# Performance work log

Hardware: AMD Instinct MI355X
Metric: run time of the kernel (lower is better)

## Reference

```python
import jax, jax.numpy as jnp
import numpy as np
from itertools import product

D = 128      # full-resolution voxel grid extent
DP = 64      # pooled grid extent (stride 2)
M = 131072   # number of pooled (output) voxels
CH = 2       # children per pooled cell
N = M * CH   # number of input active voxels = 262144
EPS = 1e-5


def _build_maps():
    rng = np.random.default_rng(0)
    plin = rng.choice(DP ** 3, size=M, replace=False).astype(np.int64)
    px = plin // (DP * DP); py = (plin // DP) % DP; pz = plin % DP
    pcoords = np.stack([px, py, pz], 1)                      # [M,3]
    off8 = np.array(list(product([0, 1], repeat=3)), np.int64)   # [8,3]
    sel = np.argsort(rng.random((M, 8)), 1)[:, :CH]          # pick 2 of 8 children
    coords = (pcoords[:, None, :] * 2 + off8[sel]).reshape(-1, 3)  # [N,3]

    def make_lookup(c, d):
        lin = (c[:, 0] * d + c[:, 1]) * d + c[:, 2]
        order = np.argsort(lin); slin = lin[order]
        def lookup(q):
            inb = np.all((q >= 0) & (q < d), 1)
            ql = (q[:, 0] * d + q[:, 1]) * d + q[:, 2]
            pos = np.searchsorted(slin, ql)
            pos_c = np.clip(pos, 0, len(slin) - 1)
            found = inb & (slin[pos_c] == ql)
            return np.where(found, order[pos_c], -1).astype(np.int32)
        return lookup

    lk_full = make_lookup(coords, D)
    lk_pool = make_lookup(pcoords, DP)
    off27 = np.array(list(product([-1, 0, 1], repeat=3)), np.int64)  # [27,3]
    nbr1 = np.stack([lk_full(coords + o) for o in off27])            # [27,N]
    pool_map = np.stack([lk_full(pcoords * 2 + o) for o in off8])    # [8,M]
    nbr2 = np.stack([lk_pool(pcoords + o) for o in off27])           # [27,M]
    return nbr1, pool_map, nbr2


def setup_inputs() -> dict:
    nbr1, pool_map, nbr2 = _build_maps()
    key = jax.random.key(0)
    k1, k2, k3, k4 = jax.random.split(key, 4)
    feats = jax.random.normal(k1, (N, 3), jnp.float32)
    # kaiming-ish scaling over fan_in = 27*Cin
    W1 = jax.random.normal(k2, (27, 3, 64), jnp.float32) * np.sqrt(2.0 / (27 * 3))
    W2 = jax.random.normal(k3, (27, 64, 64), jnp.float32) * np.sqrt(2.0 / (27 * 64))
    W3 = jax.random.normal(k4, (27, 64, 128), jnp.float32) * np.sqrt(2.0 / (27 * 64))
    return {"feats": feats, "W1": W1, "W2": W2, "W3": W3,
            "nbr1": jnp.asarray(nbr1), "pool_map": jnp.asarray(pool_map),
            "nbr2": jnp.asarray(nbr2)}


def sparse_conv(x, W, nbr):
    """Gather-GEMM-scatter sparse conv. x:[Nin,Cin], W:[K,Cin,Cout], nbr:[K,Nout]."""
    out = jnp.zeros((nbr.shape[1], W.shape[-1]), x.dtype)
    for k in range(W.shape[0]):           # fixed small loop over 27 kernel offsets
        idx = nbr[k]
        m = (idx >= 0)
        g = x[jnp.where(m, idx, 0)] * m[:, None].astype(x.dtype)  # [Nout,Cin]
        out = out + g @ W[k]
    return out


def inst_norm(x):
    mu = jnp.mean(x, axis=0, keepdims=True)
    var = jnp.var(x, axis=0, keepdims=True)
    return (x - mu) / jnp.sqrt(var + EPS)


def max_pool(x, pool_map):
    out = jnp.full((pool_map.shape[1], x.shape[1]), -jnp.inf, x.dtype)
    for o in range(pool_map.shape[0]):    # 8 pooling offsets
        idx = pool_map[o]
        m = (idx >= 0)
        g = jnp.where(m[:, None], x[jnp.where(m, idx, 0)], -jnp.inf)
        out = jnp.maximum(out, g)
    return out


def reference(feats, W1, W2, W3, nbr1, pool_map, nbr2):
    x = jax.nn.relu(inst_norm(sparse_conv(feats, W1, nbr1)))  # [N,64]
    x = jax.nn.relu(inst_norm(sparse_conv(x, W2, nbr1)))      # [N,64]
    x = max_pool(x, pool_map)                                  # [M,64]
    x = jax.nn.relu(inst_norm(sparse_conv(x, W3, nbr2)))      # [M,128]
    return x
```

## Files before the change

kernel.cpp:

```cpp
#include <hip/hip_runtime.h>
#include <hip/hip_bf16.h>

#define N_FULL 262144
#define M_POOL 131072

typedef __attribute__((ext_vector_type(4))) float f32x4;
typedef __attribute__((ext_vector_type(8))) short bf16x8;
typedef __attribute__((ext_vector_type(8))) unsigned short u16x8;

static __device__ __forceinline__ unsigned short f2b(float f) {
    __hip_bfloat16 b = __float2bfloat16(f);
    return *reinterpret_cast<unsigned short*>(&b);
}
static __device__ __forceinline__ float b2f(unsigned short u) {
    unsigned int x = ((unsigned int)u) << 16;
    return __uint_as_float(x);
}

static __device__ __forceinline__ void gll16(const void* g, void* l) {
    __builtin_amdgcn_global_load_lds(
        (const __attribute__((address_space(1))) void*)g,
        (__attribute__((address_space(3))) void*)l, 16, 0, 0);
}

template<int CT, int NPT>
__global__ __launch_bounds__(256) void pack_w_kernel(const float* __restrict__ W,
                                                     unsigned short* __restrict__ Wp) {
    int i = blockIdx.x * 256 + threadIdx.x;
    const int total = NPT * 2 * CT * 64 * 8;
    if (i >= total) return;
    int j = i & 7;
    int l = (i >> 3) & 63;
    int t = (i >> 9) % CT;
    int q = (i / (512 * CT)) & 1;
    int k = i / (1024 * CT);
    int cin = q * 32 + (l >> 4) * 8 + j;
    int cout = t * 16 + (l & 15);
    float v = (k < 27) ? W[(k * 64 + cin) * (CT * 16) + cout] : 0.f;
    Wp[i] = f2b(v);
}

__global__ __launch_bounds__(256) void pack_w1_kernel(const float* __restrict__ W1,
                                                      unsigned short* __restrict__ Wp) {
    int i = blockIdx.x * 256 + threadIdx.x;
    const int total = 7 * 4 * 64 * 8;
    if (i >= total) return;
    int j = i & 7;
    int l = (i >> 3) & 63;
    int t = (i >> 9) & 3;
    int kb = i >> 11;
    int tap = kb * 4 + (l >> 4);
    float v = 0.f;
    if (tap < 27 && j < 3) v = W1[(tap * 3 + j) * 64 + t * 16 + (l & 15)];
    Wp[i] = f2b(v);
}

__global__ __launch_bounds__(256) void conv1_mfma_kernel(const float* __restrict__ feats,
                                                         const unsigned short* __restrict__ Wp,
                                                         const int* __restrict__ nbr,
                                                         unsigned short* __restrict__ Y,
                                                         float* __restrict__ sums, int R) {
    __shared__ unsigned short lw[7 * 2048];
    __shared__ float psum[4][64], psq[4][64];
    const int tid = threadIdx.x;
    const int wave = tid >> 6;
    const int lane = tid & 63;
    const int l16 = lane & 15;
    const int lq = lane >> 4;
    const int rowbase = blockIdx.x * 128 + wave * 32;

    {
        const char* gsrc = (const char*)Wp;
        char* lbase = (char*)lw;
        #pragma unroll
        for (int c = 0; c < 7; ++c) {
            int off = (wave * 7 + c) * 1024;
            gll16(gsrc + off + lane * 16, lbase + off);
        }
    }
    int idx[7][2];
    #pragma unroll
    for (int g = 0; g < 7; ++g) {
        int tap = g * 4 + lq;
        #pragma unroll
        for (int s = 0; s < 2; ++s)
            idx[g][s] = (tap < 27) ? nbr[(size_t)tap * R + rowbase + s * 16 + l16] : -1;
    }
    __syncthreads();

    f32x4 acc[2][4];
    #pragma unroll
    for (int s = 0; s < 2; ++s)
        #pragma unroll
        for (int t = 0; t < 4; ++t)
            #pragma unroll
            for (int g = 0; g < 4; ++g) acc[s][t][g] = 0.f;
    bf16x8 zf;
    #pragma unroll
    for (int j = 0; j < 8; ++j) zf[j] = 0;

    bf16x8 af[7][2];
    #pragma unroll
    for (int g = 0; g < 7; ++g)
        #pragma unroll
        for (int s = 0; s < 2; ++s) {
            af[g][s] = zf;
            int ic = idx[g][s];
            if (ic >= 0) {
                af[g][s][0] = (short)f2b(feats[ic * 3 + 0]);
                af[g][s][1] = (short)f2b(feats[ic * 3 + 1]);
                af[g][s][2] = (short)f2b(feats[ic * 3 + 2]);
            }
        }
    #pragma unroll
    for (int g = 0; g < 7; ++g) {
        #pragma unroll
        for (int t = 0; t < 4; ++t) {
            bf16x8 bfr = *reinterpret_cast<const bf16x8*>(&lw[g * 2048 + t * 512 + lane * 8]);
            #pragma unroll
            for (int s = 0; s < 2; ++s)
                acc[s][t] = __builtin_amdgcn_mfma_f32_16x16x32_bf16(af[g][s], bfr, acc[s][t], 0, 0, 0);
        }
    }
    #pragma unroll
    for (int t = 0; t < 4; ++t) {
        float s1 = 0.f, s2 = 0.f;
        #pragma unroll
        for (int s = 0; s < 2; ++s)
            #pragma unroll
            for (int g = 0; g < 4; ++g) {
                float v = acc[s][t][g];
                s1 += v; s2 += v * v;
                Y[(size_t)(rowbase + s * 16 + lq * 4 + g) * 64 + t * 16 + l16] = f2b(v);
            }
        s1 += __shfl_xor(s1, 16); s2 += __shfl_xor(s2, 16);
        s1 += __shfl_xor(s1, 32); s2 += __shfl_xor(s2, 32);
        if (lq == 0) { psum[wave][t * 16 + l16] = s1; psq[wave][t * 16 + l16] = s2; }
    }
    __syncthreads();
    if (tid < 64) {
        float s1 = 0.f, s2 = 0.f;
        #pragma unroll
        for (int w = 0; w < 4; ++w) { s1 += psum[w][tid]; s2 += psq[w][tid]; }
        atomicAdd(&sums[tid], s1);
        atomicAdd(&sums[64 + tid], s2);
    }
}

template<int CT, int TCH, int NPT>
__global__ __launch_bounds__(256) void conv_mfma_kernel(const unsigned short* __restrict__ X,
                                                        const unsigned short* __restrict__ Wp,
                                                        const int* __restrict__ nbr,
                                                        unsigned short* __restrict__ Y,
                                                        float* __restrict__ sums, int Nout) {
    constexpr int C = CT * 16;
    constexpr int NPH = NPT / TCH;
    constexpr int TAPB = 2 * CT * 512;
    __shared__ unsigned short lw[TCH * TAPB];
    __shared__ float psum[4][C], psq[4][C];
    const int tid = threadIdx.x;
    const int wave = tid >> 6;
    const int lane = tid & 63;
    const int l16 = lane & 15;
    const int lq = lane >> 4;
    const int rowbase = blockIdx.x * 128 + wave * 32;

    f32x4 acc[2][CT];
    #pragma unroll
    for (int s = 0; s < 2; ++s)
        #pragma unroll
        for (int t = 0; t < CT; ++t)
            #pragma unroll
            for (int g = 0; g < 4; ++g) acc[s][t][g] = 0.f;
    bf16x8 zf;
    #pragma unroll
    for (int j = 0; j < 8; ++j) zf[j] = 0;

    int idxp[TCH][2];
    #pragma unroll
    for (int t = 0; t < TCH; ++t)
        #pragma unroll
        for (int s = 0; s < 2; ++s)
            idxp[t][s] = nbr[(size_t)t * Nout + rowbase + s * 16 + l16];

    for (int ph = 0; ph < NPH; ++ph) {
        if (ph) __syncthreads();
        {
            const char* gseg = (const char*)Wp + (size_t)ph * TCH * TAPB * 2;
            char* lbase = (char*)lw;
            const int woff = wave * (TCH * TAPB * 2 / 4);
            #pragma unroll
            for (int c = 0; c < TCH * CT / 2; ++c) {
                int off = woff + c * 1024;
                gll16(gseg + off + lane * 16, lbase + off);
            }
        }
        bf16x8 af[TCH][2][2];
        #pragma unroll
        for (int t = 0; t < TCH; ++t)
            #pragma unroll
            for (int s = 0; s < 2; ++s) {
                int ic = idxp[t][s];
                #pragma unroll
                for (int q = 0; q < 2; ++q) af[t][s][q] = zf;
                if (ic >= 0) {
                    #pragma unroll
                    for (int q = 0; q < 2; ++q)
                        af[t][s][q] = *reinterpret_cast<const bf16x8*>(
                            X + (size_t)ic * 64 + q * 32 + lq * 8);
                }
            }
        int idxn[TCH][2];
        #pragma unroll
        for (int t = 0; t < TCH; ++t) {
            int tap = (ph + 1) * TCH + t;
            #pragma unroll
            for (int s = 0; s < 2; ++s)
                idxn[t][s] = (tap < 27) ? nbr[(size_t)tap * Nout + rowbase + s * 16 + l16] : -1;
        }
        __syncthreads();
        #pragma unroll
        for (int t = 0; t < TCH; ++t) {
            #pragma unroll
            for (int q = 0; q < 2; ++q) {
                #pragma unroll
                for (int tt = 0; tt < CT; ++tt) {
                    bf16x8 bfr = *reinterpret_cast<const bf16x8*>(
                        &lw[t * TAPB + (q * CT + tt) * 512 + lane * 8]);
                    #pragma unroll
                    for (int s = 0; s < 2; ++s)
                        acc[s][tt] = __builtin_amdgcn_mfma_f32_16x16x32_bf16(
                            af[t][s][q], bfr, acc[s][tt], 0, 0, 0);
                }
            }
        }
        #pragma unroll
        for (int t = 0; t < TCH; ++t)
            #pragma unroll
            for (int s = 0; s < 2; ++s) idxp[t][s] = idxn[t][s];
    }
    #pragma unroll
    for (int t = 0; t < CT; ++t) {
        float s1 = 0.f, s2 = 0.f;
        #pragma unroll
        for (int s = 0; s < 2; ++s)
            #pragma unroll
            for (int g = 0; g < 4; ++g) {
                float v = acc[s][t][g];
                s1 += v; s2 += v * v;
                Y[(size_t)(rowbase + s * 16 + lq * 4 + g) * C + t * 16 + l16] = f2b(v);
            }
        s1 += __shfl_xor(s1, 16); s2 += __shfl_xor(s2, 16);
        s1 += __shfl_xor(s1, 32); s2 += __shfl_xor(s2, 32);
        if (lq == 0) { psum[wave][t * 16 + l16] = s1; psq[wave][t * 16 + l16] = s2; }
    }
    __syncthreads();
    if (tid < C) {
        float s1 = 0.f, s2 = 0.f;
        #pragma unroll
        for (int w = 0; w < 4; ++w) { s1 += psum[w][tid]; s2 += psq[w][tid]; }
        atomicAdd(&sums[tid], s1);
        atomicAdd(&sums[C + tid], s2);
    }
}

template<int C>
__global__ __launch_bounds__(256) void norm_bf16_kernel(const unsigned short* __restrict__ Y,
                                                        const float* __restrict__ sums,
                                                        unsigned short* __restrict__ Xb, int R) {
    __shared__ float lmu[C], lrs[C];
    if (threadIdx.x < C) {
        float m = sums[threadIdx.x] / (float)R;
        float v = sums[C + threadIdx.x] / (float)R - m * m;
        lmu[threadIdx.x] = m;
        lrs[threadIdx.x] = rsqrtf(fmaxf(v, 0.f) + 1e-5f);
    }
    __syncthreads();
    const int total = R * C / 8;
    for (int i = blockIdx.x * 256 + threadIdx.x; i < total; i += gridDim.x * 256) {
        u16x8 v = reinterpret_cast<const u16x8*>(Y)[i];
        int cb = (i * 8) & (C - 1);
        u16x8 o;
        #pragma unroll
        for (int j = 0; j < 8; ++j) {
            float f = b2f(v[j]);
            o[j] = f2b(fmaxf((f - lmu[cb + j]) * lrs[cb + j], 0.f));
        }
        reinterpret_cast<u16x8*>(Xb)[i] = o;
    }
}

template<int C>
__global__ __launch_bounds__(256) void norm_f32_kernel(const unsigned short* __restrict__ Y,
                                                       const float* __restrict__ sums,
                                                       float* __restrict__ Out, int R) {
    __shared__ float lmu[C], lrs[C];
    if (threadIdx.x < C) {
        float m = sums[threadIdx.x] / (float)R;
        float v = sums[C + threadIdx.x] / (float)R - m * m;
        lmu[threadIdx.x] = m;
        lrs[threadIdx.x] = rsqrtf(fmaxf(v, 0.f) + 1e-5f);
    }
    __syncthreads();
    const int total = R * C / 8;
    for (int i = blockIdx.x * 256 + threadIdx.x; i < total; i += gridDim.x * 256) {
        u16x8 v = reinterpret_cast<const u16x8*>(Y)[i];
        int cb = (i * 8) & (C - 1);
        float4 o0, o1;
        o0.x = fmaxf((b2f(v[0]) - lmu[cb + 0]) * lrs[cb + 0], 0.f);
        o0.y = fmaxf((b2f(v[1]) - lmu[cb + 1]) * lrs[cb + 1], 0.f);
        o0.z = fmaxf((b2f(v[2]) - lmu[cb + 2]) * lrs[cb + 2], 0.f);
        o0.w = fmaxf((b2f(v[3]) - lmu[cb + 3]) * lrs[cb + 3], 0.f);
        o1.x = fmaxf((b2f(v[4]) - lmu[cb + 4]) * lrs[cb + 4], 0.f);
        o1.y = fmaxf((b2f(v[5]) - lmu[cb + 5]) * lrs[cb + 5], 0.f);
        o1.z = fmaxf((b2f(v[6]) - lmu[cb + 6]) * lrs[cb + 6], 0.f);
        o1.w = fmaxf((b2f(v[7]) - lmu[cb + 7]) * lrs[cb + 7], 0.f);
        reinterpret_cast<float4*>(Out)[i * 2] = o0;
        reinterpret_cast<float4*>(Out)[i * 2 + 1] = o1;
    }
}

__global__ __launch_bounds__(256) void pool_norm_kernel(const unsigned short* __restrict__ Y2,
                                                        const int* __restrict__ pmap,
                                                        const float* __restrict__ sums,
                                                        unsigned short* __restrict__ Xp,
                                                        int M, int R) {
    __shared__ float lmu[64], lrs[64];
    if (threadIdx.x < 64) {
        float m = sums[threadIdx.x] / (float)R;
        float v = sums[64 + threadIdx.x] / (float)R - m * m;
        lmu[threadIdx.x] = m;
        lrs[threadIdx.x] = rsqrtf(fmaxf(v, 0.f) + 1e-5f);
    }
    __syncthreads();
    const int lane = threadIdx.x & 63;
    const int gw = blockIdx.x * 4 + (threadIdx.x >> 6);
    const int nw = gridDim.x * 4;
    for (int m = gw; m < M; m += nw) {
        int idx[8];
        #pragma unroll
        for (int o = 0; o < 8; ++o) idx[o] = pmap[o * M + m];
        float best = -INFINITY;
        #pragma unroll
        for (int o = 0; o < 8; ++o)
            if (idx[o] >= 0) best = fmaxf(best, b2f(Y2[(size_t)idx[o] * 64 + lane]));
        Xp[(size_t)m * 64 + lane] = f2b(fmaxf((best - lmu[lane]) * lrs[lane], 0.f));
    }
}

extern "C" void kernel_launch(void* const* d_in, const int* in_sizes, int n_in,
                              void* d_out, int out_size, void* d_ws, size_t ws_size,
                              hipStream_t stream) {
    const float* feats = (const float*)d_in[0];
    const float* W1 = (const float*)d_in[1];
    const float* W2 = (const float*)d_in[2];
    const float* W3 = (const float*)d_in[3];
    const int* nbr1 = (const int*)d_in[4];
    const int* pmap = (const int*)d_in[5];
    const int* nbr2 = (const int*)d_in[6];
    float* out = (float*)d_out;

    const int N = N_FULL, M = M_POOL;
    char* ws = (char*)d_ws;
    unsigned short* yb = (unsigned short*)ws;
    unsigned short* xb = yb + (size_t)N * 64;
    unsigned short* w1p = xb + (size_t)N * 64;
    unsigned short* w2p = w1p + 7 * 4 * 64 * 8;
    unsigned short* w3p = w2p + 30 * 2 * 4 * 512;
    float* sums = (float*)(w3p + 27 * 2 * 8 * 512);
    float* sums1 = sums;
    float* sums2 = sums + 128;
    float* sums3 = sums + 256;

    hipMemsetAsync(sums, 0, 512 * sizeof(float), stream);
    pack_w1_kernel<<<(7 * 2048 + 255) / 256, 256, 0, stream>>>(W1, w1p);
    pack_w_kernel<4, 30><<<(30 * 4096 + 255) / 256, 256, 0, stream>>>(W2, w2p);
    pack_w_kernel<8, 27><<<(27 * 8192 + 255) / 256, 256, 0, stream>>>(W3, w3p);

    conv1_mfma_kernel<<<N / 128, 256, 0, stream>>>(feats, w1p, nbr1, yb, sums1, N);
    norm_bf16_kernel<64><<<2048, 256, 0, stream>>>(yb, sums1, xb, N);

    conv_mfma_kernel<4, 6, 30><<<N / 128, 256, 0, stream>>>(xb, w2p, nbr1, yb, sums2, N);
    pool_norm_kernel<<<2048, 256, 0, stream>>>(yb, pmap, sums2, xb, M, N);

    conv_mfma_kernel<8, 3, 27><<<M / 128, 256, 0, stream>>>(xb, w3p, nbr2, yb, sums3, M);
    norm_f32_kernel<128><<<2048, 256, 0, stream>>>(yb, sums3, out, M);
}
```

Before: 386.1 us.

## Double-buffer weight staging and prefetch gathers one phase ahead in sparse conv

Restructures the conv2/conv3 MFMA kernel into a software pipeline. Weight segments are double-buffered in LDS and the next phase's neighbor indices and feature gathers are issued before the current phase's MFMAs, with explicit vmcnt waits and raw barriers in place of full syncthreads. Missing neighbors are redirected to a zeroed sentinel row, removing the per-row branch, and tap chunking is retuned to fewer taps per phase with padding to 28 taps. This trades more registers (two sets of A fragments) and an extra padded tap of work for latency hiding of the gather loads.

```diff
diff --git a/kernel.cpp b/kernel.cpp
--- a/kernel.cpp
+++ b/kernel.cpp
@@ -55,6 +55,10 @@
     Wp[i] = f2b(v);
 }
 
+__global__ void zero_row_kernel(unsigned short* __restrict__ xb) {
+    if (threadIdx.x < 64) xb[(size_t)N_FULL * 64 + threadIdx.x] = 0;
+}
+
 __global__ __launch_bounds__(256) void conv1_mfma_kernel(const float* __restrict__ feats,
                                                          const unsigned short* __restrict__ Wp,
                                                          const int* __restrict__ nbr,
@@ -152,11 +156,15 @@
                                                         const unsigned short* __restrict__ Wp,
                                                         const int* __restrict__ nbr,
                                                         unsigned short* __restrict__ Y,
-                                                        float* __restrict__ sums, int Nout) {
+                                                        float* __restrict__ sums,
+                                                        int Nout, int zrow) {
     constexpr int C = CT * 16;
     constexpr int NPH = NPT / TCH;
-    constexpr int TAPB = 2 * CT * 512;
-    __shared__ unsigned short lw[TCH * TAPB];
+    constexpr int TAPW = CT * 1024;
+    constexpr int PHW = TCH * TAPW;
+    constexpr int SCH = TCH * CT / 2;
+    constexpr int VM = TCH * 6;
+    __shared__ unsigned short lw[2][PHW];
     __shared__ float psum[4][C], psq[4][C];
     const int tid = threadIdx.x;
     const int wave = tid >> 6;
@@ -172,73 +180,87 @@
         for (int t = 0; t < CT; ++t)
             #pragma unroll
             for (int g = 0; g < 4; ++g) acc[s][t][g] = 0.f;
-    bf16x8 zf;
-    #pragma unroll
-    for (int j = 0; j < 8; ++j) zf[j] = 0;
-
-    int idxp[TCH][2];
-    #pragma unroll
-    for (int t = 0; t < TCH; ++t)
-        #pragma unroll
-        for (int s = 0; s < 2; ++s)
-            idxp[t][s] = nbr[(size_t)t * Nout + rowbase + s * 16 + l16];
-
-    for (int ph = 0; ph < NPH; ++ph) {
-        if (ph) __syncthreads();
-        {
-            const char* gseg = (const char*)Wp + (size_t)ph * TCH * TAPB * 2;
-            char* lbase = (char*)lw;
-            const int woff = wave * (TCH * TAPB * 2 / 4);
-            #pragma unroll
-            for (int c = 0; c < TCH * CT / 2; ++c) {
-                int off = woff + c * 1024;
-                gll16(gseg + off + lane * 16, lbase + off);
+
+    auto stage = [&](unsigned short* dst, int seg) {
+        const char* g = (const char*)(Wp + (size_t)seg * PHW);
+        char* l = (char*)dst;
+        const int woff = wave * (SCH * 1024);
+        #pragma unroll
+        for (int c = 0; c < SCH; ++c) {
+            int off = woff + c * 1024;
+            gll16(g + off + lane * 16, l + off);
+        }
+    };
+    auto gatherA = [&](bf16x8 (&af)[TCH][2][2], const int (&id)[TCH][2]) {
+        #pragma unroll
+        for (int t = 0; t < TCH; ++t)
+            #pragma unroll
+            for (int s = 0; s < 2; ++s) {
+                int ic = id[t][s] < 0 ? zrow : id[t][s];
+                const unsigned short* base = X + (size_t)ic * 64 + lq * 8;
+                af[t][s][0] = *reinterpret_cast<const bf16x8*>(base);
+                af[t][s][1] = *reinterpret_cast<const bf16x8*>(base + 32);
             }
-        }
-        bf16x8 af[TCH][2][2];
+    };
+    auto loadIdx = [&](int (&id)[TCH][2], int ph2) {
+        #pragma unroll
+        for (int t = 0; t < TCH; ++t) {
+            int tap = ph2 * TCH + t;
+            if (tap > 26) tap = 26;
+            #pragma unroll
+            for (int s = 0; s < 2; ++s)
+                id[t][s] = nbr[(size_t)tap * Nout + rowbase + s * 16 + l16];
+        }
+    };
+    auto compute = [&](const unsigned short* buf, const bf16x8 (&af)[TCH][2][2]) {
+        __builtin_amdgcn_s_setprio(1);
         #pragma unroll
         for (int t = 0; t < TCH; ++t)
             #pragma unroll
-            for (int s = 0; s < 2; ++s) {
-                int ic = idxp[t][s];
-                #pragma unroll
-                for (int q = 0; q < 2; ++q) af[t][s][q] = zf;
-                if (ic >= 0) {
-                    #pragma unroll
-                    for (int q = 0; q < 2; ++q)
-                        af[t][s][q] = *reinterpret_cast<const bf16x8*>(
-                            X + (size_t)ic * 64 + q * 32 + lq * 8);
-                }
-            }
-        int idxn[TCH][2];
-        #pragma unroll
-        for (int t = 0; t < TCH; ++t) {
-            int tap = (ph + 1) * TCH + t;
-            #pragma unroll
-            for (int s = 0; s < 2; ++s)
-                idxn[t][s] = (tap < 27) ? nbr[(size_t)tap * Nout + rowbase + s * 16 + l16] : -1;
-        }
-        __syncthreads();
-        #pragma unroll
-        for (int t = 0; t < TCH; ++t) {
-            #pragma unroll
-            for (int q = 0; q < 2; ++q) {
+            for (int q = 0; q < 2; ++q)
                 #pragma unroll
                 for (int tt = 0; tt < CT; ++tt) {
-                    bf16x8 bfr = *reinterpret_cast<const bf16x8*>(
-                        &lw[t * TAPB + (q * CT + tt) * 512 + lane * 8]);
+                    bf16x8 b = *reinterpret_cast<const bf16x8*>(
+                        &buf[t * TAPW + (q * CT + tt) * 512 + lane * 8]);
                     #pragma unroll
                     for (int s = 0; s < 2; ++s)
                         acc[s][tt] = __builtin_amdgcn_mfma_f32_16x16x32_bf16(
-                            af[t][s][q], bfr, acc[s][tt], 0, 0, 0);
+                            af[t][s][q], b, acc[s][tt], 0, 0, 0);
                 }
-            }
-        }
-        #pragma unroll
-        for (int t = 0; t < TCH; ++t)
-            #pragma unroll
-            for (int s = 0; s < 2; ++s) idxp[t][s] = idxn[t][s];
-    }
+        __builtin_amdgcn_s_setprio(0);
+    };
+    auto body = [&](int ph, const unsigned short* bufc, unsigned short* bufn,
+                    const bf16x8 (&afc)[TCH][2][2], bf16x8 (&afn)[TCH][2][2],
+                    const int (&idu)[TCH][2], int (&idw)[TCH][2]) {
+        int seg = ph + 1; if (seg > NPH - 1) seg = NPH - 1;
+        stage(bufn, seg);
+        asm volatile("" ::: "memory");
+        gatherA(afn, idu);
+        loadIdx(idw, ph + 2);
+        compute(bufc, afc);
+        if constexpr (VM == 6)
+            asm volatile("s_waitcnt vmcnt(6)" ::: "memory");
+        else if constexpr (VM == 12)
+            asm volatile("s_waitcnt vmcnt(12)" ::: "memory");
+        else
+            asm volatile("s_waitcnt vmcnt(0)" ::: "memory");
+        __builtin_amdgcn_s_barrier();
+        asm volatile("" ::: "memory");
+    };
+
+    int id0[TCH][2], id1[TCH][2];
+    bf16x8 af0[TCH][2][2], af1[TCH][2][2];
+    stage((unsigned short*)lw[0], 0);
+    loadIdx(id0, 0);
+    gatherA(af0, id0);
+    loadIdx(id0, 1);
+    __syncthreads();
+
+    for (int ph = 0; ph < NPH; ph += 2) {
+        body(ph,     (unsigned short*)lw[0], (unsigned short*)lw[1], af0, af1, id0, id1);
+        body(ph + 1, (unsigned short*)lw[1], (unsigned short*)lw[0], af1, af0, id1, id0);
+    }
+
     #pragma unroll
     for (int t = 0; t < CT; ++t) {
         float s1 = 0.f, s2 = 0.f;
@@ -364,25 +386,26 @@
     char* ws = (char*)d_ws;
     unsigned short* yb = (unsigned short*)ws;
     unsigned short* xb = yb + (size_t)N * 64;
-    unsigned short* w1p = xb + (size_t)N * 64;
-    unsigned short* w2p = w1p + 7 * 4 * 64 * 8;
-    unsigned short* w3p = w2p + 30 * 2 * 4 * 512;
-    float* sums = (float*)(w3p + 27 * 2 * 8 * 512);
+    unsigned short* w1p = xb + (size_t)(N + 1) * 64;
+    unsigned short* w2p = w1p + 7 * 2048;
+    unsigned short* w3p = w2p + 28 * 4096;
+    float* sums = (float*)(w3p + 28 * 8192);
     float* sums1 = sums;
     float* sums2 = sums + 128;
     float* sums3 = sums + 256;
 
     hipMemsetAsync(sums, 0, 512 * sizeof(float), stream);
+    zero_row_kernel<<<1, 64, 0, stream>>>(xb);
     pack_w1_kernel<<<(7 * 2048 + 255) / 256, 256, 0, stream>>>(W1, w1p);
-    pack_w_kernel<4, 30><<<(30 * 4096 + 255) / 256, 256, 0, stream>>>(W2, w2p);
-    pack_w_kernel<8, 27><<<(27 * 8192 + 255) / 256, 256, 0, stream>>>(W3, w3p);
+    pack_w_kernel<4, 28><<<(28 * 4096 + 255) / 256, 256, 0, stream>>>(W2, w2p);
+    pack_w_kernel<8, 28><<<(28 * 8192 + 255) / 256, 256, 0, stream>>>(W3, w3p);
 
     conv1_mfma_kernel<<<N / 128, 256, 0, stream>>>(feats, w1p, nbr1, yb, sums1, N);
     norm_bf16_kernel<64><<<2048, 256, 0, stream>>>(yb, sums1, xb, N);
 
-    conv_mfma_kernel<4, 6, 30><<<N / 128, 256, 0, stream>>>(xb, w2p, nbr1, yb, sums2, N);
+    conv_mfma_kernel<4, 2, 28><<<N / 128, 256, 0, stream>>>(xb, w2p, nbr1, yb, sums2, N, N);
     pool_norm_kernel<<<2048, 256, 0, stream>>>(yb, pmap, sums2, xb, M, N);
 
-    conv_mfma_kernel<8, 3, 27><<<M / 128, 256, 0, stream>>>(xb, w3p, nbr2, yb, sums3, M);
+    conv_mfma_kernel<8, 1, 28><<<M / 128, 256, 0, stream>>>(xb, w3p, nbr2, yb, sums3, M, N);
     norm_f32_kernel<128><<<2048, 256, 0, stream>>>(yb, sums3, out, M);
 }
```

Result: slower. 413.4 us (+7.1%).

## Use 512-thread conv blocks and branchless gathers via a zero sentinel row

Applied to the files above, without the earlier changes.

Doubles the conv blocks to 8 waves (256 rows per block), so each staged weight phase in LDS is shared by twice as many rows and the per-wave copy share is halved. Missing neighbours are remapped to a zeroed sentinel row, which makes feature gathers unconditional vector loads instead of branches. Conv1 input is prepacked to 4-wide bf16 rows so each gather is a single 8-byte load. The larger blocks may lower occupancy and add register pressure, and the extra prep kernels add a little launch overhead.

```diff
diff --git a/kernel.cpp b/kernel.cpp
--- a/kernel.cpp
+++ b/kernel.cpp
@@ -43,7 +43,7 @@
 __global__ __launch_bounds__(256) void pack_w1_kernel(const float* __restrict__ W1,
                                                       unsigned short* __restrict__ Wp) {
     int i = blockIdx.x * 256 + threadIdx.x;
-    const int total = 7 * 4 * 64 * 8;
+    const int total = 8 * 4 * 64 * 8;
     if (i >= total) return;
     int j = i & 7;
     int l = (i >> 3) & 63;
@@ -55,37 +55,67 @@
     Wp[i] = f2b(v);
 }
 
-__global__ __launch_bounds__(256) void conv1_mfma_kernel(const float* __restrict__ feats,
+__global__ __launch_bounds__(256) void pack_feats_kernel(const float* __restrict__ feats,
+                                                         unsigned short* __restrict__ fp, int N) {
+    int i = blockIdx.x * 256 + threadIdx.x;
+    if (i > N) return;
+    ushort4 o;
+    if (i < N) {
+        o.x = f2b(feats[(size_t)i * 3 + 0]);
+        o.y = f2b(feats[(size_t)i * 3 + 1]);
+        o.z = f2b(feats[(size_t)i * 3 + 2]);
+        o.w = 0;
+    } else { o.x = o.y = o.z = o.w = 0; }
+    reinterpret_cast<ushort4*>(fp)[i] = o;
+}
+
+__global__ void zero_row_kernel(unsigned short* __restrict__ xb) {
+    if (threadIdx.x < 64) xb[(size_t)N_FULL * 64 + threadIdx.x] = 0;
+}
+
+__global__ __launch_bounds__(512) void conv1_mfma_kernel(const unsigned short* __restrict__ fp,
                                                          const unsigned short* __restrict__ Wp,
                                                          const int* __restrict__ nbr,
                                                          unsigned short* __restrict__ Y,
                                                          float* __restrict__ sums, int R) {
-    __shared__ unsigned short lw[7 * 2048];
-    __shared__ float psum[4][64], psq[4][64];
+    __shared__ unsigned short lw[8 * 2048];
+    __shared__ float psum[8][64], psq[8][64];
     const int tid = threadIdx.x;
     const int wave = tid >> 6;
     const int lane = tid & 63;
     const int l16 = lane & 15;
     const int lq = lane >> 4;
-    const int rowbase = blockIdx.x * 128 + wave * 32;
+    const int rowbase = blockIdx.x * 256 + wave * 32;
+    const int zrow = R;
 
     {
         const char* gsrc = (const char*)Wp;
         char* lbase = (char*)lw;
         #pragma unroll
-        for (int c = 0; c < 7; ++c) {
-            int off = (wave * 7 + c) * 1024;
+        for (int c = 0; c < 4; ++c) {
+            int off = (wave * 4 + c) * 1024;
             gll16(gsrc + off + lane * 16, lbase + off);
         }
     }
     int idx[7][2];
     #pragma unroll
     for (int g = 0; g < 7; ++g) {
-        int tap = g * 4 + lq;
-        #pragma unroll
-        for (int s = 0; s < 2; ++s)
-            idx[g][s] = (tap < 27) ? nbr[(size_t)tap * R + rowbase + s * 16 + l16] : -1;
-    }
+        int tap = g * 4 + lq; if (tap > 26) tap = 26;
+        #pragma unroll
+        for (int s = 0; s < 2; ++s) {
+            int v = nbr[(size_t)tap * R + rowbase + s * 16 + l16];
+            idx[g][s] = v < 0 ? zrow : v;
+        }
+    }
+    bf16x8 af[7][2];
+    #pragma unroll
+    for (int g = 0; g < 7; ++g)
+        #pragma unroll
+        for (int s = 0; s < 2; ++s) {
+            short4 v = *reinterpret_cast<const short4*>(fp + (size_t)idx[g][s] * 4);
+            af[g][s][0] = v.x; af[g][s][1] = v.y; af[g][s][2] = v.z; af[g][s][3] = v.w;
+            af[g][s][4] = 0; af[g][s][5] = 0; af[g][s][6] = 0; af[g][s][7] = 0;
+        }
     __syncthreads();
 
     f32x4 acc[2][4];
@@ -95,23 +125,7 @@
         for (int t = 0; t < 4; ++t)
             #pragma unroll
             for (int g = 0; g < 4; ++g) acc[s][t][g] = 0.f;
-    bf16x8 zf;
-    #pragma unroll
-    for (int j = 0; j < 8; ++j) zf[j] = 0;
-
-    bf16x8 af[7][2];
-    #pragma unroll
-    for (int g = 0; g < 7; ++g)
-        #pragma unroll
-        for (int s = 0; s < 2; ++s) {
-            af[g][s] = zf;
-            int ic = idx[g][s];
-            if (ic >= 0) {
-                af[g][s][0] = (short)f2b(feats[ic * 3 + 0]);
-                af[g][s][1] = (short)f2b(feats[ic * 3 + 1]);
-                af[g][s][2] = (short)f2b(feats[ic * 3 + 2]);
-            }
-        }
+
     #pragma unroll
     for (int g = 0; g < 7; ++g) {
         #pragma unroll
@@ -141,29 +155,32 @@
     if (tid < 64) {
         float s1 = 0.f, s2 = 0.f;
         #pragma unroll
-        for (int w = 0; w < 4; ++w) { s1 += psum[w][tid]; s2 += psq[w][tid]; }
+        for (int w = 0; w < 8; ++w) { s1 += psum[w][tid]; s2 += psq[w][tid]; }
         atomicAdd(&sums[tid], s1);
         atomicAdd(&sums[64 + tid], s2);
     }
 }
 
 template<int CT, int TCH, int NPT>
-__global__ __launch_bounds__(256) void conv_mfma_kernel(const unsigned short* __restrict__ X,
+__global__ __launch_bounds__(512) void conv_mfma_kernel(const unsigned short* __restrict__ X,
                                                         const unsigned short* __restrict__ Wp,
                                                         const int* __restrict__ nbr,
                                                         unsigned short* __restrict__ Y,
-                                                        float* __restrict__ sums, int Nout) {
+                                                        float* __restrict__ sums,
+                                                        int Nout, int zrow) {
     constexpr int C = CT * 16;
     constexpr int NPH = NPT / TCH;
-    constexpr int TAPB = 2 * CT * 512;
-    __shared__ unsigned short lw[TCH * TAPB];
-    __shared__ float psum[4][C], psq[4][C];
+    constexpr int TAPW = CT * 1024;
+    constexpr int PHW = TCH * TAPW;
+    constexpr int SCH = TCH * CT / 4;
+    __shared__ unsigned short lw[PHW];
+    __shared__ float psum[8][C], psq[8][C];
     const int tid = threadIdx.x;
     const int wave = tid >> 6;
     const int lane = tid & 63;
     const int l16 = lane & 15;
     const int lq = lane >> 4;
-    const int rowbase = blockIdx.x * 128 + wave * 32;
+    const int rowbase = blockIdx.x * 256 + wave * 32;
 
     f32x4 acc[2][CT];
     #pragma unroll
@@ -172,25 +189,24 @@
         for (int t = 0; t < CT; ++t)
             #pragma unroll
             for (int g = 0; g < 4; ++g) acc[s][t][g] = 0.f;
-    bf16x8 zf;
-    #pragma unroll
-    for (int j = 0; j < 8; ++j) zf[j] = 0;
 
     int idxp[TCH][2];
     #pragma unroll
     for (int t = 0; t < TCH; ++t)
         #pragma unroll
-        for (int s = 0; s < 2; ++s)
-            idxp[t][s] = nbr[(size_t)t * Nout + rowbase + s * 16 + l16];
+        for (int s = 0; s < 2; ++s) {
+            int v = nbr[(size_t)t * Nout + rowbase + s * 16 + l16];
+            idxp[t][s] = v < 0 ? zrow : v;
+        }
 
     for (int ph = 0; ph < NPH; ++ph) {
         if (ph) __syncthreads();
         {
-            const char* gseg = (const char*)Wp + (size_t)ph * TCH * TAPB * 2;
+            const char* gseg = (const char*)(Wp + (size_t)ph * PHW);
             char* lbase = (char*)lw;
-            const int woff = wave * (TCH * TAPB * 2 / 4);
-            #pragma unroll
-            for (int c = 0; c < TCH * CT / 2; ++c) {
+            const int woff = wave * (SCH * 1024);
+            #pragma unroll
+            for (int c = 0; c < SCH; ++c) {
                 int off = woff + c * 1024;
                 gll16(gseg + off + lane * 16, lbase + off);
             }
@@ -200,40 +216,34 @@
         for (int t = 0; t < TCH; ++t)
             #pragma unroll
             for (int s = 0; s < 2; ++s) {
-                int ic = idxp[t][s];
-                #pragma unroll
-                for (int q = 0; q < 2; ++q) af[t][s][q] = zf;
-                if (ic >= 0) {
-                    #pragma unroll
-                    for (int q = 0; q < 2; ++q)
-                        af[t][s][q] = *reinterpret_cast<const bf16x8*>(
-                            X + (size_t)ic * 64 + q * 32 + lq * 8);
-                }
+                const unsigned short* base = X + (size_t)idxp[t][s] * 64 + lq * 8;
+                af[t][s][0] = *reinterpret_cast<const bf16x8*>(base);
+                af[t][s][1] = *reinterpret_cast<const bf16x8*>(base + 32);
             }
         int idxn[TCH][2];
         #pragma unroll
         for (int t = 0; t < TCH; ++t) {
-            int tap = (ph + 1) * TCH + t;
-            #pragma unroll
-            for (int s = 0; s < 2; ++s)
-                idxn[t][s] = (tap < 27) ? nbr[(size_t)tap * Nout + rowbase + s * 16 + l16] : -1;
+            int tap = (ph + 1) * TCH + t; if (tap > 26) tap = 26;
+            #pragma unroll
+            for (int s = 0; s < 2; ++s) {
+                int v = nbr[(size_t)tap * Nout + rowbase + s * 16 + l16];
+                idxn[t][s] = v < 0 ? zrow : v;
+            }
         }
         __syncthreads();
         #pragma unroll
-        for (int t = 0; t < TCH; ++t) {
-            #pragma unroll
-            for (int q = 0; q < 2; ++q) {
+        for (int t = 0; t < TCH; ++t)
+            #pragma unroll
+            for (int q = 0; q < 2; ++q)
                 #pragma unroll
                 for (int tt = 0; tt < CT; ++tt) {
                     bf16x8 bfr = *reinterpret_cast<const bf16x8*>(
-                        &lw[t * TAPB + (q * CT + tt) * 512 + lane * 8]);
+                        &lw[t * TAPW + (q * CT + tt) * 512 + lane * 8]);
                     #pragma unroll
                     for (int s = 0; s < 2; ++s)
                         acc[s][tt] = __builtin_amdgcn_mfma_f32_16x16x32_bf16(
                             af[t][s][q], bfr, acc[s][tt], 0, 0, 0);
                 }
-            }
-        }
         #pragma unroll
         for (int t = 0; t < TCH; ++t)
             #pragma unroll
@@ -258,7 +268,7 @@
     if (tid < C) {
         float s1 = 0.f, s2 = 0.f;
         #pragma unroll
-        for (int w = 0; w < 4; ++w) { s1 += psum[w][tid]; s2 += psq[w][tid]; }
+        for (int w = 0; w < 8; ++w) { s1 += psum[w][tid]; s2 += psq[w][tid]; }
         atomicAdd(&sums[tid], s1);
         atomicAdd(&sums[C + tid], s2);
     }
@@ -364,25 +374,28 @@
     char* ws = (char*)d_ws;
     unsigned short* yb = (unsigned short*)ws;
     unsigned short* xb = yb + (size_t)N * 64;
-    unsigned short* w1p = xb + (size_t)N * 64;
-    unsigned short* w2p = w1p + 7 * 4 * 64 * 8;
-    unsigned short* w3p = w2p + 30 * 2 * 4 * 512;
-    float* sums = (float*)(w3p + 27 * 2 * 8 * 512);
+    unsigned short* fpk = xb + (size_t)(N + 1) * 64;
+    unsigned short* w1p = fpk + (size_t)(N + 1) * 4;
+    unsigned short* w2p = w1p + 8 * 2048;
+    unsigned short* w3p = w2p + 30 * 4096;
+    float* sums = (float*)(w3p + 27 * 8192);
     float* sums1 = sums;
     float* sums2 = sums + 128;
     float* sums3 = sums + 256;
 
     hipMemsetAsync(sums, 0, 512 * sizeof(float), stream);
-    pack_w1_kernel<<<(7 * 2048 + 255) / 256, 256, 0, stream>>>(W1, w1p);
+    zero_row_kernel<<<1, 64, 0, stream>>>(xb);
+    pack_feats_kernel<<<(N + 256) / 256, 256, 0, stream>>>(feats, fpk, N);
+    pack_w1_kernel<<<(8 * 2048 + 255) / 256, 256, 0, stream>>>(W1, w1p);
     pack_w_kernel<4, 30><<<(30 * 4096 + 255) / 256, 256, 0, stream>>>(W2, w2p);
     pack_w_kernel<8, 27><<<(27 * 8192 + 255) / 256, 256, 0, stream>>>(W3, w3p);
 
-    conv1_mfma_kernel<<<N / 128, 256, 0, stream>>>(feats, w1p, nbr1, yb, sums1, N);
+    conv1_mfma_kernel<<<N / 256, 512, 0, stream>>>(fpk, w1p, nbr1, yb, sums1, N);
     norm_bf16_kernel<64><<<2048, 256, 0, stream>>>(yb, sums1, xb, N);
 
-    conv_mfma_kernel<4, 6, 30><<<N / 128, 256, 0, stream>>>(xb, w2p, nbr1, yb, sums2, N);
+    conv_mfma_kernel<4, 6, 30><<<N / 256, 512, 0, stream>>>(xb, w2p, nbr1, yb, sums2, N, N);
     pool_norm_kernel<<<2048, 256, 0, stream>>>(yb, pmap, sums2, xb, M, N);
 
-    conv_mfma_kernel<8, 3, 27><<<M / 128, 256, 0, stream>>>(xb, w3p, nbr2, yb, sums3, M);
+    conv_mfma_kernel<8, 3, 27><<<M / 256, 512, 0, stream>>>(xb, w3p, nbr2, yb, sums3, M, N);
     norm_f32_kernel<128><<<2048, 256, 0, stream>>>(yb, sums3, out, M);
 }
```

Result: slower. 412.6 us (+6.9%).
